# Performance work log

Measured on AMD Instinct MI355X. Metric: run time of the kernel, lower is better.

## Reference

```python
import jax, jax.numpy as jnp
import numpy as np

EMBED = 512
HEADS = 8
HEAD_D = EMBED // HEADS
N = 16
QLEN = 512
KLEN = 512


def _relative_keys(Wr, q_len, k_len):
    # Transformer-XL style sinusoid table of size (q_len + k_len)
    max_dist = q_len + k_len
    inv_freqs = 10000.0 ** (-jnp.arange(0, EMBED, 2, dtype=jnp.float32) / EMBED)
    seq = jnp.arange(max_dist, dtype=jnp.float32)[:, None] * inv_freqs[None, :]
    pos_emb = jnp.concatenate([jnp.sin(seq), jnp.cos(seq)], axis=-1)  # [max_dist, E]
    rel = (pos_emb @ Wr.T).reshape(max_dist, HEADS, HEAD_D)           # [max_dist, H, D]
    # query_offset defaults to key_len
    q_pos = jnp.arange(q_len)[:, None] + k_len
    k_pos = jnp.arange(k_len)[None, :]
    rel_idx = jnp.clip(q_pos - k_pos, 0, max_dist - 1)                # [q, k]
    return rel[rel_idx]                                               # [q, k, H, D]


def setup_inputs() -> dict:
    key = jax.random.key(0)
    ks = jax.random.split(key, 12)
    s = 0.02
    return {
        "values": jax.random.normal(ks[0], (N, KLEN, EMBED), jnp.float32),
        "keys": jax.random.normal(ks[1], (N, KLEN, EMBED), jnp.float32),
        "query": jax.random.normal(ks[2], (N, QLEN, EMBED), jnp.float32),
        "mask": jnp.ones((N, QLEN, KLEN), jnp.int32),
        "Wv": jax.random.normal(ks[3], (HEAD_D, HEAD_D), jnp.float32) * s,
        "Wk": jax.random.normal(ks[4], (HEAD_D, HEAD_D), jnp.float32) * s,
        "Wq": jax.random.normal(ks[5], (HEAD_D, HEAD_D), jnp.float32) * s,
        "Wr": jax.random.normal(ks[6], (EMBED, EMBED), jnp.float32) * s,
        "u_bias": jax.random.normal(ks[7], (HEADS, HEAD_D), jnp.float32) * s,
        "v_bias": jax.random.normal(ks[8], (HEADS, HEAD_D), jnp.float32) * s,
        "Wo": jax.random.normal(ks[9], (EMBED, EMBED), jnp.float32) * s,
        "bo": jnp.zeros((EMBED,), jnp.float32),
    }


def reference(values, keys, query, mask, Wv, Wk, Wq, Wr, u_bias, v_bias, Wo, bo):
    # per-head projections (same D x D weight shared across heads, torch Linear: x @ W.T)
    v = values.reshape(N, KLEN, HEADS, HEAD_D) @ Wv.T
    k = keys.reshape(N, KLEN, HEADS, HEAD_D) @ Wk.T
    q = query.reshape(N, QLEN, HEADS, HEAD_D) @ Wq.T

    rel_keys = _relative_keys(Wr, QLEN, KLEN)  # [q, k, H, D]

    content = jnp.einsum("nqhd,nkhd->nhqk", q + u_bias, k)
    position = jnp.einsum("nqhd,qkhd->nhqk", q + v_bias, rel_keys)
    energy = content + position
    energy = jnp.where(mask[:, None, :, :] == 0, jnp.float32(-1e20), energy)

    attn = jax.nn.softmax(energy / (float(HEAD_D) ** 0.5), axis=3)  # [N,H,q,k]
    out = jnp.einsum("nhqk,nkhd->nqhd", attn, v).reshape(N, QLEN, EMBED)
    out = out @ Wo.T + bo
    return out, attn
```

## Files before the change

kernel.cpp:

```cpp
#include <hip/hip_runtime.h>
#include <math.h>

#define NB     16
#define HEADS  8
#define HD     64
#define EMBED  512
#define QL     512
#define KL     512

#define WS_QU   0
#define WS_QV   2097152
#define WS_KB   4194304
#define WS_VT   6291456
#define WS_PEB  8388608
#define WS_RELB 8912896
#define WS_OH   9175040

typedef __attribute__((ext_vector_type(8))) short bf16x8;
typedef __attribute__((ext_vector_type(4))) float f32x4;
typedef __attribute__((ext_vector_type(8))) unsigned short ushort8v;
typedef __attribute__((ext_vector_type(4))) unsigned short ushort4v;

#define MFMA16 __builtin_amdgcn_mfma_f32_16x16x32_bf16

static __device__ __forceinline__ unsigned short f2bf(float x) {
    unsigned u = __builtin_bit_cast(unsigned, x);
    u += 0x7fffu + ((u >> 16) & 1u);
    return (unsigned short)(u >> 16);
}

static __device__ __forceinline__ float bf2f(unsigned short v) {
    unsigned u = ((unsigned)v) << 16;
    return __builtin_bit_cast(float, u);
}

__global__ void pe_kernel(unsigned short* __restrict__ peb) {
    int j = blockIdx.x;
    int i = threadIdx.x;
    float invf = exp2f(-(float)i * (13.287712379549449f / 256.0f));
    float ang  = (float)j * invf;
    peb[j * 512 + i]       = f2bf(sinf(ang));
    peb[j * 512 + 256 + i] = f2bf(cosf(ang));
}

__global__ __launch_bounds__(256) void rel_kernel(const unsigned short* __restrict__ peb,
                                                  const float* __restrict__ Wr,
                                                  unsigned short* __restrict__ relb) {
    __shared__ __align__(16) unsigned short At[64][64];
    __shared__ __align__(16) unsigned short Bt[64][64];
    int bm = blockIdx.x >> 3, bn = blockIdx.x & 7;
    int tid = threadIdx.x;
    int w = tid >> 6, lane = tid & 63;
    int fr = lane & 15, fg = lane >> 4;
    f32x4 acc[4] = {};
    for (int kk = 0; kk < 512; kk += 64) {
        __syncthreads();
        for (int p = 0; p < 2; ++p) {
            int idx = tid + 256 * p;
            int row = idx >> 3, slot = idx & 7;
            *(bf16x8*)&At[row][((slot ^ (row & 7))) * 8] =
                *(const bf16x8*)&peb[(bm * 64 + row) * 512 + kk + slot * 8];
        }
        for (int p = 0; p < 4; ++p) {
            int idx = tid + 256 * p;
            int row = idx >> 4, c4 = idx & 15;
            float4 v = *(const float4*)&Wr[(bn * 64 + row) * 512 + kk + c4 * 4];
            ushort4v pk;
            pk[0] = f2bf(v.x); pk[1] = f2bf(v.y); pk[2] = f2bf(v.z); pk[3] = f2bf(v.w);
            int slot = c4 >> 1, rem = (c4 & 1) * 4;
            *(ushort4v*)&Bt[row][((slot ^ (row & 7))) * 8 + rem] = pk;
        }
        __syncthreads();
        bf16x8 af[2];
        int ar = w * 16 + fr;
#pragma unroll
        for (int s = 0; s < 2; ++s)
            af[s] = *(const bf16x8*)&At[ar][((fg + 4 * s) ^ (ar & 7)) * 8];
#pragma unroll
        for (int c = 0; c < 4; ++c) {
            int br = c * 16 + fr;
#pragma unroll
            for (int s = 0; s < 2; ++s) {
                bf16x8 bf = *(const bf16x8*)&Bt[br][((fg + 4 * s) ^ (br & 7)) * 8];
                acc[c] = MFMA16(af[s], bf, acc[c], 0, 0, 0);
            }
        }
    }
#pragma unroll
    for (int c = 0; c < 4; ++c)
#pragma unroll
        for (int i = 0; i < 4; ++i)
            relb[(bn * 1024 + bm * 64 + w * 16 + fg * 4 + i) * 64 + c * 16 + fr] =
                f2bf(acc[c][i]);
}

__global__ __launch_bounds__(256) void proj_kernel(const float* __restrict__ query,
                                                   const float* __restrict__ keys,
                                                   const float* __restrict__ values,
                                                   const float* __restrict__ Wq,
                                                   const float* __restrict__ Wk,
                                                   const float* __restrict__ Wv,
                                                   const float* __restrict__ u_bias,
                                                   const float* __restrict__ v_bias,
                                                   float* __restrict__ ws) {
    __shared__ __align__(16) unsigned short inb[32][512];
    __shared__ __align__(16) unsigned short Wb[3][64][64];
    __shared__ __align__(16) unsigned short vtile[4][64][36];
    int n = blockIdx.x >> 4, t0 = (blockIdx.x & 15) * 32;
    int tid = threadIdx.x;
    int w = tid >> 6, lane = tid & 63;
    int fr = lane & 15, fg = lane >> 4;

    for (int p = 0; p < 3; ++p) {
        const float* Wp = (p == 0) ? Wq : (p == 1) ? Wk : Wv;
        for (int it = 0; it < 4; ++it) {
            int idx = tid + 256 * it;
            int row = idx >> 4, c4 = idx & 15;
            float4 v = *(const float4*)&Wp[row * 64 + c4 * 4];
            ushort4v pk;
            pk[0] = f2bf(v.x); pk[1] = f2bf(v.y); pk[2] = f2bf(v.z); pk[3] = f2bf(v.w);
            int slot = c4 >> 1, rem = (c4 & 1) * 4;
            *(ushort4v*)&Wb[p][row][((slot ^ (row & 7))) * 8 + rem] = pk;
        }
    }
    unsigned short* qu_b = (unsigned short*)(ws + WS_QU);
    unsigned short* qv_b = (unsigned short*)(ws + WS_QV);
    unsigned short* k_b  = (unsigned short*)(ws + WS_KB);
    unsigned short* vT_b = (unsigned short*)(ws + WS_VT);

    for (int p = 0; p < 3; ++p) {
        const float* src = (p == 0) ? query : (p == 1) ? keys : values;
        __syncthreads();
        for (int it = 0; it < 16; ++it) {
            int idx = tid + 256 * it;
            int row = idx >> 7, c4 = idx & 127;
            float4 v = *(const float4*)&src[((long)(n * 512 + t0 + row)) * 512 + c4 * 4];
            ushort4v pk;
            pk[0] = f2bf(v.x); pk[1] = f2bf(v.y); pk[2] = f2bf(v.z); pk[3] = f2bf(v.w);
            int slot = c4 >> 1, rem = (c4 & 1) * 4;
            *(ushort4v*)&inb[row][((slot ^ (row & 7))) * 8 + rem] = pk;
        }
        __syncthreads();
        for (int hh = 0; hh < 2; ++hh) {
            int h = w * 2 + hh, nh = n * 8 + h;
            bf16x8 af[2][2];
#pragma unroll
            for (int tt = 0; tt < 2; ++tt) {
                int ar = tt * 16 + fr;
#pragma unroll
                for (int s = 0; s < 2; ++s)
                    af[tt][s] = *(const bf16x8*)&inb[ar][(h * 8 + ((fg + 4 * s) ^ (ar & 7))) * 8];
            }
            f32x4 acc[2][4] = {};
#pragma unroll
            for (int dt = 0; dt < 4; ++dt) {
                int br = dt * 16 + fr;
                bf16x8 bf[2];
#pragma unroll
                for (int s = 0; s < 2; ++s)
                    bf[s] = *(const bf16x8*)&Wb[p][br][((fg + 4 * s) ^ (br & 7)) * 8];
#pragma unroll
                for (int tt = 0; tt < 2; ++tt)
#pragma unroll
                    for (int s = 0; s < 2; ++s)
                        acc[tt][dt] = MFMA16(af[tt][s], bf[s], acc[tt][dt], 0, 0, 0);
            }
            if (p == 0) {
#pragma unroll
                for (int dt = 0; dt < 4; ++dt) {
                    float ub = u_bias[h * 64 + dt * 16 + fr];
                    float vb = v_bias[h * 64 + dt * 16 + fr];
#pragma unroll
                    for (int tt = 0; tt < 2; ++tt)
#pragma unroll
                        for (int i = 0; i < 4; ++i) {
                            long o = ((long)(nh * 512 + t0 + tt * 16 + fg * 4 + i)) * 64 +
                                     dt * 16 + fr;
                            qu_b[o] = f2bf(acc[tt][dt][i] + ub);
                            qv_b[o] = f2bf(acc[tt][dt][i] + vb);
                        }
                }
            } else if (p == 1) {
#pragma unroll
                for (int dt = 0; dt < 4; ++dt)
#pragma unroll
                    for (int tt = 0; tt < 2; ++tt)
#pragma unroll
                        for (int i = 0; i < 4; ++i)
                            k_b[((long)(nh * 512 + t0 + tt * 16 + fg * 4 + i)) * 64 +
                                dt * 16 + fr] = f2bf(acc[tt][dt][i]);
            } else {
#pragma unroll
                for (int dt = 0; dt < 4; ++dt)
#pragma unroll
                    for (int tt = 0; tt < 2; ++tt)
#pragma unroll
                        for (int i = 0; i < 4; ++i)
                            vtile[w][dt * 16 + fr][tt * 16 + fg * 4 + i] =
                                f2bf(acc[tt][dt][i]);
                __syncthreads();
#pragma unroll
                for (int dg = 0; dg < 8; ++dg) {
                    int d = dg * 8 + (lane >> 3), tq = lane & 7;
                    *(ushort4v*)&vT_b[((long)(nh * 64 + d)) * 512 + t0 + tq * 4] =
                        *(const ushort4v*)&vtile[w][d][tq * 4];
                }
                __syncthreads();
            }
        }
    }
}

__global__ __launch_bounds__(512) void attn_kernel(float* __restrict__ ws,
                                                   const int* __restrict__ mask,
                                                   float* __restrict__ d_out) {
    __shared__ __align__(16) float S[32][520];
    __shared__ __align__(16) float red[4][32][17];

    const unsigned short* qu_b = (const unsigned short*)(ws + WS_QU);
    const unsigned short* qv_b = (const unsigned short*)(ws + WS_QV);
    const unsigned short* k_b  = (const unsigned short*)(ws + WS_KB);
    const unsigned short* vT_b = (const unsigned short*)(ws + WS_VT);
    const unsigned short* relb = (const unsigned short*)(ws + WS_RELB);
    unsigned short* ohb = (unsigned short*)(ws + WS_OH);
    float* attn = d_out + 4194304;

    int bid = blockIdx.x;
    int swz = (bid & 7) * 128 + (bid >> 3);
    int nh = swz >> 3, qg = swz & 7;
    int n  = nh >> 3, h = nh & 7;

    int tid  = threadIdx.x;
    int w    = tid >> 6, lane = tid & 63;
    int fr   = lane & 15, fg = lane >> 4;

    const unsigned short* kbase = k_b + (long)nh * 512 * 64;
    bf16x8 kreg[4][2];
#pragma unroll
    for (int t = 0; t < 4; ++t) {
        const unsigned short* kp = kbase + (long)(w * 64 + t * 16 + fr) * 64;
        kreg[t][0] = *(const bf16x8*)&kp[fg * 8];
        kreg[t][1] = *(const bf16x8*)&kp[(fg + 4) * 8];
    }
    int dt = w & 3, kh = w >> 2;
    const unsigned short* vp0 = vT_b + ((long)(nh * 64 + dt * 16 + fr)) * 512 + kh * 256;
    bf16x8 vreg[8];
#pragma unroll
    for (int kk = 0; kk < 8; ++kk)
        vreg[kk] = *(const bf16x8*)&vp0[kk * 32 + fg * 8];

    const unsigned short* rbase = relb + (long)h * 1024 * 64;
    int jt0 = 28 - 4 * w;

    for (int ti = 0; ti < 2; ++ti) {
        int q0 = qg * 64 + ti * 32;

        {
            bf16x8 qvf[2][2];
#pragma unroll
            for (int qt = 0; qt < 2; ++qt) {
                long qa = ((long)(nh * 512 + q0 + qt * 16 + fr)) * 64;
                qvf[qt][0] = *(const bf16x8*)&qv_b[qa + fg * 8];
                qvf[qt][1] = *(const bf16x8*)&qv_b[qa + (fg + 4) * 8];
            }
#pragma unroll
            for (int pp = 0; pp < 3; ++pp) {
                int jjA = (jt0 + 2 * pp) * 16 + fr;
                int jjB = jjA + 16;
                int jA = q0 + 1 + jjA; if (jA > 1023) jA = 1023;
                int jB = q0 + 1 + jjB; if (jB > 1023) jB = 1023;
                const unsigned short* rpA = rbase + (long)jA * 64;
                const unsigned short* rpB = rbase + (long)jB * 64;
                bf16x8 a0 = *(const bf16x8*)&rpA[fg * 8];
                bf16x8 a1 = *(const bf16x8*)&rpA[(fg + 4) * 8];
                bf16x8 c0 = *(const bf16x8*)&rpB[fg * 8];
                bf16x8 c1 = *(const bf16x8*)&rpB[(fg + 4) * 8];
                __builtin_amdgcn_s_setprio(1);
#pragma unroll
                for (int qt = 0; qt < 2; ++qt) {
                    f32x4 accA = {0.f, 0.f, 0.f, 0.f};
                    f32x4 accB = {0.f, 0.f, 0.f, 0.f};
                    accA = MFMA16(qvf[qt][0], a0, accA, 0, 0, 0);
                    accA = MFMA16(qvf[qt][1], a1, accA, 0, 0, 0);
                    accB = MFMA16(qvf[qt][0], c0, accB, 0, 0, 0);
                    accB = MFMA16(qvf[qt][1], c1, accB, 0, 0, 0);
#pragma unroll
                    for (int i = 0; i < 4; ++i) {
                        int r = qt * 16 + fg * 4 + i;
                        int kA = r + 511 - jjA;
                        int kB = r + 511 - jjB;
                        if ((unsigned)(kA - w * 64) < 64u)
                            S[r][kA ^ (4 * (r & 7))] = accA[i];
                        if ((unsigned)(kB - w * 64) < 64u)
                            S[r][kB ^ (4 * (r & 7))] = accB[i];
                    }
                }
                __builtin_amdgcn_s_setprio(0);
            }
        }

        {
            bf16x8 qf[2][2];
#pragma unroll
            for (int qt = 0; qt < 2; ++qt) {
                long qa = ((long)(nh * 512 + q0 + qt * 16 + fr)) * 64;
                qf[qt][0] = *(const bf16x8*)&qu_b[qa + fg * 8];
                qf[qt][1] = *(const bf16x8*)&qu_b[qa + (fg + 4) * 8];
            }
            __builtin_amdgcn_s_setprio(1);
#pragma unroll
            for (int t = 0; t < 4; ++t) {
#pragma unroll
                for (int qt = 0; qt < 2; ++qt) {
                    f32x4* sp = (f32x4*)&S[qt * 16 + fr]
                                        [(w * 64 + t * 16 + fg * 4) ^ (4 * (fr & 7))];
                    f32x4 acc = *sp;
                    acc = MFMA16(kreg[t][0], qf[qt][0], acc, 0, 0, 0);
                    acc = MFMA16(kreg[t][1], qf[qt][1], acc, 0, 0, 0);
                    *sp = acc;
                }
            }
            __builtin_amdgcn_s_setprio(0);
        }
        __syncthreads();

        for (int rr = 0; rr < 4; ++rr) {
            int r = w * 4 + rr;
            int x4 = 4 * (r & 7), x8 = 8 * (r & 7);
            const int* mrow = mask + ((long)(n * 512 + q0 + r)) * 512;
            float lg[8];
            float mx = -3.0e38f;
#pragma unroll
            for (int j = 0; j < 8; ++j) {
                int k = lane + 64 * j;
                float s = S[r][k ^ x4];
                int m = mrow[k];
                float l = (m == 0) ? -1.25e19f : s * 0.125f;
                lg[j] = l;
                mx = fmaxf(mx, l);
            }
            for (int o = 32; o > 0; o >>= 1) mx = fmaxf(mx, __shfl_xor(mx, o, 64));
            float sum = 0.f;
#pragma unroll
            for (int j = 0; j < 8; ++j) { lg[j] = __expf(lg[j] - mx); sum += lg[j]; }
            for (int o = 32; o > 0; o >>= 1) sum += __shfl_xor(sum, o, 64);
            float inv = 1.0f / sum;
            unsigned short* prow = (unsigned short*)&S[r][0];
            float* arow = attn + ((long)(nh * 512 + q0 + r)) * 512;
#pragma unroll
            for (int j = 0; j < 8; ++j) {
                int k = lane + 64 * j;
                float p = lg[j] * inv;
                prow[k ^ x8] = f2bf(p);
                arow[k] = p;
            }
        }
        __syncthreads();

        {
            f32x4 oacc[2] = {{0.f,0.f,0.f,0.f},{0.f,0.f,0.f,0.f}};
            __builtin_amdgcn_s_setprio(1);
#pragma unroll
            for (int kk = 0; kk < 8; ++kk) {
#pragma unroll
                for (int qt = 0; qt < 2; ++qt) {
                    int row = qt * 16 + fr;
                    const unsigned short* prow = (const unsigned short*)&S[row][0];
                    bf16x8 pf = *(const bf16x8*)
                        &prow[(kh * 256 + kk * 32 + fg * 8) ^ (8 * (row & 7))];
                    oacc[qt] = MFMA16(pf, vreg[kk], oacc[qt], 0, 0, 0);
                }
            }
            __builtin_amdgcn_s_setprio(0);
            if (kh == 1) {
#pragma unroll
                for (int qt = 0; qt < 2; ++qt)
#pragma unroll
                    for (int i = 0; i < 4; ++i)
                        red[dt][qt * 16 + fg * 4 + i][fr] = oacc[qt][i];
            }
            __syncthreads();
            if (kh == 0) {
#pragma unroll
                for (int qt = 0; qt < 2; ++qt)
#pragma unroll
                    for (int i = 0; i < 4; ++i) {
                        float o = oacc[qt][i] + red[dt][qt * 16 + fg * 4 + i][fr];
                        ohb[((long)(n * 512 + q0 + qt * 16 + fg * 4 + i)) * 512 +
                            h * 64 + dt * 16 + fr] = f2bf(o);
                    }
            }
        }
    }
}

__global__ __launch_bounds__(256) void wo_kernel(const float* __restrict__ ws,
                                                 const float* __restrict__ Wo,
                                                 const float* __restrict__ bo,
                                                 float* __restrict__ d_out) {
    __shared__ __align__(16) unsigned short At[128][64];
    __shared__ __align__(16) unsigned short Bt[64][64];
    const unsigned short* ohb = (const unsigned short*)(ws + WS_OH);
    int bm = blockIdx.x >> 3, bn = blockIdx.x & 7;
    int tid = threadIdx.x;
    int w = tid >> 6, lane = tid & 63;
    int fr = lane & 15, fg = lane >> 4;
    f32x4 acc[2][4] = {};
    for (int kk = 0; kk < 512; kk += 64) {
        __syncthreads();
        for (int p = 0; p < 4; ++p) {
            int idx = tid + 256 * p;
            int row = idx >> 3, slot = idx & 7;
            *(bf16x8*)&At[row][((slot ^ (row & 7))) * 8] =
                *(const bf16x8*)&ohb[(long)(bm * 128 + row) * 512 + kk + slot * 8];
        }
        for (int p = 0; p < 2; ++p) {
            int idx = tid + 256 * p;
            int row = idx >> 3, slot = idx & 7;
            const float* g = &Wo[(bn * 64 + row) * 512 + kk + slot * 8];
            float4 a = *(const float4*)g;
            float4 b = *(const float4*)(g + 4);
            ushort8v pk;
            pk[0] = f2bf(a.x); pk[1] = f2bf(a.y); pk[2] = f2bf(a.z); pk[3] = f2bf(a.w);
            pk[4] = f2bf(b.x); pk[5] = f2bf(b.y); pk[6] = f2bf(b.z); pk[7] = f2bf(b.w);
            *(ushort8v*)&Bt[row][((slot ^ (row & 7))) * 8] = pk;
        }
        __syncthreads();
        bf16x8 af[2][2], bfr[4][2];
#pragma unroll
        for (int t = 0; t < 2; ++t) {
            int ar = w * 32 + t * 16 + fr;
#pragma unroll
            for (int s = 0; s < 2; ++s)
                af[t][s] = *(const bf16x8*)&At[ar][((fg + s * 4) ^ (ar & 7)) * 8];
        }
#pragma unroll
        for (int c = 0; c < 4; ++c) {
            int br = c * 16 + fr;
#pragma unroll
            for (int s = 0; s < 2; ++s)
                bfr[c][s] = *(const bf16x8*)&Bt[br][((fg + s * 4) ^ (br & 7)) * 8];
        }
#pragma unroll
        for (int t = 0; t < 2; ++t)
#pragma unroll
            for (int c = 0; c < 4; ++c)
#pragma unroll
                for (int s = 0; s < 2; ++s)
                    acc[t][c] = MFMA16(af[t][s], bfr[c][s], acc[t][c], 0, 0, 0);
    }
#pragma unroll
    for (int t = 0; t < 2; ++t)
#pragma unroll
        for (int c = 0; c < 4; ++c) {
            int col = bn * 64 + c * 16 + fr;
            float b = bo[col];
#pragma unroll
            for (int i = 0; i < 4; ++i) {
                int row = bm * 128 + w * 32 + t * 16 + fg * 4 + i;
                d_out[(long)row * 512 + col] = acc[t][c][i] + b;
            }
        }
}

extern "C" void kernel_launch(void* const* d_in, const int* in_sizes, int n_in,
                              void* d_out, int out_size, void* d_ws, size_t ws_size,
                              hipStream_t stream) {
    const float* values = (const float*)d_in[0];
    const float* keys   = (const float*)d_in[1];
    const float* query  = (const float*)d_in[2];
    const int*   mask   = (const int*)d_in[3];
    const float* Wv     = (const float*)d_in[4];
    const float* Wk     = (const float*)d_in[5];
    const float* Wq     = (const float*)d_in[6];
    const float* Wr     = (const float*)d_in[7];
    const float* u_bias = (const float*)d_in[8];
    const float* v_bias = (const float*)d_in[9];
    const float* Wo     = (const float*)d_in[10];
    const float* bo     = (const float*)d_in[11];
    float* out = (float*)d_out;
    float* ws  = (float*)d_ws;

    unsigned short* peb  = (unsigned short*)(ws + WS_PEB);
    unsigned short* relb = (unsigned short*)(ws + WS_RELB);

    hipLaunchKernelGGL(pe_kernel,   dim3(1024),  dim3(256), 0, stream, peb);
    hipLaunchKernelGGL(rel_kernel,  dim3(128),   dim3(256), 0, stream, peb, Wr, relb);
    hipLaunchKernelGGL(proj_kernel, dim3(256),   dim3(256), 0, stream,
                       query, keys, values, Wq, Wk, Wv, u_bias, v_bias, ws);
    hipLaunchKernelGGL(attn_kernel, dim3(1024),  dim3(512), 0, stream, ws, mask, out);
    hipLaunchKernelGGL(wo_kernel,   dim3(512),   dim3(256), 0, stream, ws, Wo, bo, out);
}
```

Measured before the change: 157.6 us.

## Double-buffer bf16 score tiles and overlap PV with next tile's scores

Result: no change. 158.2 us (+0.4%).

```diff
diff --git a/kernel.cpp b/kernel.cpp
--- a/kernel.cpp
+++ b/kernel.cpp
@@ -32,6 +32,15 @@
 static __device__ __forceinline__ float bf2f(unsigned short v) {
     unsigned u = ((unsigned)v) << 16;
     return __builtin_bit_cast(float, u);
+}
+
+static __device__ __forceinline__ bf16x8 pack8(f32x4 a, f32x4 b) {
+    union { bf16x8 v; unsigned u[4]; } r;
+    asm("v_cvt_pk_bf16_f32 %0, %1, %2" : "=v"(r.u[0]) : "v"(a[0]), "v"(a[1]));
+    asm("v_cvt_pk_bf16_f32 %0, %1, %2" : "=v"(r.u[1]) : "v"(a[2]), "v"(a[3]));
+    asm("v_cvt_pk_bf16_f32 %0, %1, %2" : "=v"(r.u[2]) : "v"(b[0]), "v"(b[1]));
+    asm("v_cvt_pk_bf16_f32 %0, %1, %2" : "=v"(r.u[3]) : "v"(b[2]), "v"(b[3]));
+    return r.v;
 }
 
 __global__ void pe_kernel(unsigned short* __restrict__ peb) {
@@ -214,7 +223,7 @@
 __global__ __launch_bounds__(512) void attn_kernel(float* __restrict__ ws,
                                                    const int* __restrict__ mask,
                                                    float* __restrict__ d_out) {
-    __shared__ __align__(16) float S[32][520];
+    __shared__ __align__(16) unsigned short S16[2][32][528];
     __shared__ __align__(16) float red[4][32][17];
 
     const unsigned short* qu_b = (const unsigned short*)(ws + WS_QU);
@@ -252,146 +261,160 @@
     const unsigned short* rbase = relb + (long)h * 1024 * 64;
     int jt0 = 28 - 4 * w;
 
-    for (int ti = 0; ti < 2; ++ti) {
-        int q0 = qg * 64 + ti * 32;
-
-        {
-            bf16x8 qvf[2][2];
+    auto pos_content = [&](int q0, unsigned short (*SB)[528]) {
+        bf16x8 qf[2][2], qv[2][2];
+#pragma unroll
+        for (int qt = 0; qt < 2; ++qt) {
+            long qa = ((long)(nh * 512 + q0 + qt * 16 + fr)) * 64;
+            qf[qt][0] = *(const bf16x8*)&qu_b[qa + fg * 8];
+            qf[qt][1] = *(const bf16x8*)&qu_b[qa + (fg + 4) * 8];
+            qv[qt][0] = *(const bf16x8*)&qv_b[qa + fg * 8];
+            qv[qt][1] = *(const bf16x8*)&qv_b[qa + (fg + 4) * 8];
+        }
+#pragma unroll
+        for (int pp = 0; pp < 3; ++pp) {
+            int jtA = jt0 + 2 * pp, jtB = jtA + 1;
+            int jA = q0 + 1 + jtA * 16 + fr; if (jA > 1023) jA = 1023;
+            int jB = q0 + 1 + jtB * 16 + fr; if (jB > 1023) jB = 1023;
+            const unsigned short* rpA = rbase + (long)jA * 64;
+            const unsigned short* rpB = rbase + (long)jB * 64;
+            bf16x8 a0 = *(const bf16x8*)&rpA[fg * 8];
+            bf16x8 a1 = *(const bf16x8*)&rpA[(fg + 4) * 8];
+            bf16x8 c0 = *(const bf16x8*)&rpB[fg * 8];
+            bf16x8 c1 = *(const bf16x8*)&rpB[(fg + 4) * 8];
+            __builtin_amdgcn_s_setprio(1);
 #pragma unroll
             for (int qt = 0; qt < 2; ++qt) {
-                long qa = ((long)(nh * 512 + q0 + qt * 16 + fr)) * 64;
-                qvf[qt][0] = *(const bf16x8*)&qv_b[qa + fg * 8];
-                qvf[qt][1] = *(const bf16x8*)&qv_b[qa + (fg + 4) * 8];
-            }
-#pragma unroll
-            for (int pp = 0; pp < 3; ++pp) {
-                int jjA = (jt0 + 2 * pp) * 16 + fr;
-                int jjB = jjA + 16;
-                int jA = q0 + 1 + jjA; if (jA > 1023) jA = 1023;
-                int jB = q0 + 1 + jjB; if (jB > 1023) jB = 1023;
-                const unsigned short* rpA = rbase + (long)jA * 64;
-                const unsigned short* rpB = rbase + (long)jB * 64;
-                bf16x8 a0 = *(const bf16x8*)&rpA[fg * 8];
-                bf16x8 a1 = *(const bf16x8*)&rpA[(fg + 4) * 8];
-                bf16x8 c0 = *(const bf16x8*)&rpB[fg * 8];
-                bf16x8 c1 = *(const bf16x8*)&rpB[(fg + 4) * 8];
-                __builtin_amdgcn_s_setprio(1);
-#pragma unroll
-                for (int qt = 0; qt < 2; ++qt) {
-                    f32x4 accA = {0.f, 0.f, 0.f, 0.f};
-                    f32x4 accB = {0.f, 0.f, 0.f, 0.f};
-                    accA = MFMA16(qvf[qt][0], a0, accA, 0, 0, 0);
-                    accA = MFMA16(qvf[qt][1], a1, accA, 0, 0, 0);
-                    accB = MFMA16(qvf[qt][0], c0, accB, 0, 0, 0);
-                    accB = MFMA16(qvf[qt][1], c1, accB, 0, 0, 0);
-#pragma unroll
-                    for (int i = 0; i < 4; ++i) {
-                        int r = qt * 16 + fg * 4 + i;
-                        int kA = r + 511 - jjA;
-                        int kB = r + 511 - jjB;
-                        if ((unsigned)(kA - w * 64) < 64u)
-                            S[r][kA ^ (4 * (r & 7))] = accA[i];
-                        if ((unsigned)(kB - w * 64) < 64u)
-                            S[r][kB ^ (4 * (r & 7))] = accB[i];
-                    }
+                f32x4 accA = {0.f, 0.f, 0.f, 0.f};
+                f32x4 accB = {0.f, 0.f, 0.f, 0.f};
+                accA = MFMA16(a0, qv[qt][0], accA, 0, 0, 0);
+                accA = MFMA16(a1, qv[qt][1], accA, 0, 0, 0);
+                accB = MFMA16(c0, qv[qt][0], accB, 0, 0, 0);
+                accB = MFMA16(c1, qv[qt][1], accB, 0, 0, 0);
+                int qr = qt * 16 + fr;
+                int x8 = 8 * (fr & 7);
+#pragma unroll
+                for (int i = 0; i < 4; ++i) {
+                    int kA = qr + 511 - (jtA * 16 + fg * 4 + i);
+                    int kB = qr + 511 - (jtB * 16 + fg * 4 + i);
+                    if ((unsigned)(kA - w * 64) < 64u)
+                        SB[qr][kA ^ x8] = f2bf(accA[i]);
+                    if ((unsigned)(kB - w * 64) < 64u)
+                        SB[qr][kB ^ x8] = f2bf(accB[i]);
                 }
-                __builtin_amdgcn_s_setprio(0);
-            }
-        }
-
-        {
-            bf16x8 qf[2][2];
+            }
+            __builtin_amdgcn_s_setprio(0);
+        }
+        __builtin_amdgcn_s_setprio(1);
+#pragma unroll
+        for (int t = 0; t < 4; ++t) {
 #pragma unroll
             for (int qt = 0; qt < 2; ++qt) {
-                long qa = ((long)(nh * 512 + q0 + qt * 16 + fr)) * 64;
-                qf[qt][0] = *(const bf16x8*)&qu_b[qa + fg * 8];
-                qf[qt][1] = *(const bf16x8*)&qu_b[qa + (fg + 4) * 8];
-            }
-            __builtin_amdgcn_s_setprio(1);
-#pragma unroll
-            for (int t = 0; t < 4; ++t) {
-#pragma unroll
-                for (int qt = 0; qt < 2; ++qt) {
-                    f32x4* sp = (f32x4*)&S[qt * 16 + fr]
-                                        [(w * 64 + t * 16 + fg * 4) ^ (4 * (fr & 7))];
-                    f32x4 acc = *sp;
-                    acc = MFMA16(kreg[t][0], qf[qt][0], acc, 0, 0, 0);
-                    acc = MFMA16(kreg[t][1], qf[qt][1], acc, 0, 0, 0);
-                    *sp = acc;
-                }
-            }
-            __builtin_amdgcn_s_setprio(0);
-        }
-        __syncthreads();
-
+                int qr = qt * 16 + fr;
+                unsigned short* sp =
+                    &SB[qr][(w * 64 + t * 16 + fg * 4) ^ (8 * (fr & 7))];
+                ushort4v cv = *(ushort4v*)sp;
+                f32x4 cin = {bf2f(cv[0]), bf2f(cv[1]), bf2f(cv[2]), bf2f(cv[3])};
+                cin = MFMA16(kreg[t][0], qf[qt][0], cin, 0, 0, 0);
+                cin = MFMA16(kreg[t][1], qf[qt][1], cin, 0, 0, 0);
+                ushort4v ov;
+                ov[0] = f2bf(cin[0]); ov[1] = f2bf(cin[1]);
+                ov[2] = f2bf(cin[2]); ov[3] = f2bf(cin[3]);
+                *(ushort4v*)sp = ov;
+            }
+        }
+        __builtin_amdgcn_s_setprio(0);
+    };
+
+    auto softmax_f = [&](int q0, unsigned short (*SB)[528]) {
         for (int rr = 0; rr < 4; ++rr) {
             int r = w * 4 + rr;
-            int x4 = 4 * (r & 7), x8 = 8 * (r & 7);
-            const int* mrow = mask + ((long)(n * 512 + q0 + r)) * 512;
+            int slot = lane ^ (r & 7);
+            bf16x8 sv = *(const bf16x8*)&SB[r][slot * 8];
+            const int* mrow = mask + ((long)(n * 512 + q0 + r)) * 512 + lane * 8;
+            int4 m0 = *(const int4*)mrow;
+            int4 m1 = *(const int4*)(mrow + 4);
+            int mv[8] = {m0.x, m0.y, m0.z, m0.w, m1.x, m1.y, m1.z, m1.w};
             float lg[8];
             float mx = -3.0e38f;
 #pragma unroll
-            for (int j = 0; j < 8; ++j) {
-                int k = lane + 64 * j;
-                float s = S[r][k ^ x4];
-                int m = mrow[k];
-                float l = (m == 0) ? -1.25e19f : s * 0.125f;
-                lg[j] = l;
+            for (int u = 0; u < 8; ++u) {
+                float sraw = bf2f((unsigned short)sv[u]);
+                float l = (mv[u] == 0) ? -1.25e19f : sraw * 0.125f;
+                lg[u] = l;
                 mx = fmaxf(mx, l);
             }
             for (int o = 32; o > 0; o >>= 1) mx = fmaxf(mx, __shfl_xor(mx, o, 64));
             float sum = 0.f;
 #pragma unroll
-            for (int j = 0; j < 8; ++j) { lg[j] = __expf(lg[j] - mx); sum += lg[j]; }
+            for (int u = 0; u < 8; ++u) { lg[u] = __expf(lg[u] - mx); sum += lg[u]; }
             for (int o = 32; o > 0; o >>= 1) sum += __shfl_xor(sum, o, 64);
             float inv = 1.0f / sum;
-            unsigned short* prow = (unsigned short*)&S[r][0];
-            float* arow = attn + ((long)(nh * 512 + q0 + r)) * 512;
-#pragma unroll
-            for (int j = 0; j < 8; ++j) {
-                int k = lane + 64 * j;
-                float p = lg[j] * inv;
-                prow[k ^ x8] = f2bf(p);
-                arow[k] = p;
-            }
-        }
-        __syncthreads();
-
-        {
-            f32x4 oacc[2] = {{0.f,0.f,0.f,0.f},{0.f,0.f,0.f,0.f}};
-            __builtin_amdgcn_s_setprio(1);
-#pragma unroll
-            for (int kk = 0; kk < 8; ++kk) {
-#pragma unroll
-                for (int qt = 0; qt < 2; ++qt) {
-                    int row = qt * 16 + fr;
-                    const unsigned short* prow = (const unsigned short*)&S[row][0];
-                    bf16x8 pf = *(const bf16x8*)
-                        &prow[(kh * 256 + kk * 32 + fg * 8) ^ (8 * (row & 7))];
-                    oacc[qt] = MFMA16(pf, vreg[kk], oacc[qt], 0, 0, 0);
+            f32x4 p0 = {lg[0] * inv, lg[1] * inv, lg[2] * inv, lg[3] * inv};
+            f32x4 p1 = {lg[4] * inv, lg[5] * inv, lg[6] * inv, lg[7] * inv};
+            *(bf16x8*)&SB[r][slot * 8] = pack8(p0, p1);
+            float* arow = attn + ((long)(nh * 512 + q0 + r)) * 512 + lane * 8;
+            *(f32x4*)arow = p0;
+            *(f32x4*)(arow + 4) = p1;
+        }
+    };
+
+    auto pv = [&](unsigned short (*SB)[528], f32x4* oacc) {
+        __builtin_amdgcn_s_setprio(1);
+#pragma unroll
+        for (int kk = 0; kk < 8; ++kk) {
+#pragma unroll
+            for (int qt = 0; qt < 2; ++qt) {
+                int row = qt * 16 + fr;
+                bf16x8 pf = *(const bf16x8*)
+                    &SB[row][(kh * 256 + kk * 32 + fg * 8) ^ (8 * (fr & 7))];
+                oacc[qt] = MFMA16(pf, vreg[kk], oacc[qt], 0, 0, 0);
+            }
+        }
+        __builtin_amdgcn_s_setprio(0);
+    };
+
+    auto red_write = [&](f32x4* oacc) {
+        if (kh == 1) {
+#pragma unroll
+            for (int qt = 0; qt < 2; ++qt)
+#pragma unroll
+                for (int i = 0; i < 4; ++i)
+                    red[dt][qt * 16 + fg * 4 + i][fr] = oacc[qt][i];
+        }
+    };
+    auto red_read_store = [&](int q0, f32x4* oacc) {
+        if (kh == 0) {
+#pragma unroll
+            for (int qt = 0; qt < 2; ++qt)
+#pragma unroll
+                for (int i = 0; i < 4; ++i) {
+                    float o = oacc[qt][i] + red[dt][qt * 16 + fg * 4 + i][fr];
+                    ohb[((long)(n * 512 + q0 + qt * 16 + fg * 4 + i)) * 512 +
+                        h * 64 + dt * 16 + fr] = f2bf(o);
                 }
-            }
-            __builtin_amdgcn_s_setprio(0);
-            if (kh == 1) {
-#pragma unroll
-                for (int qt = 0; qt < 2; ++qt)
-#pragma unroll
-                    for (int i = 0; i < 4; ++i)
-                        red[dt][qt * 16 + fg * 4 + i][fr] = oacc[qt][i];
-            }
-            __syncthreads();
-            if (kh == 0) {
-#pragma unroll
-                for (int qt = 0; qt < 2; ++qt)
-#pragma unroll
-                    for (int i = 0; i < 4; ++i) {
-                        float o = oacc[qt][i] + red[dt][qt * 16 + fg * 4 + i][fr];
-                        ohb[((long)(n * 512 + q0 + qt * 16 + fg * 4 + i)) * 512 +
-                            h * 64 + dt * 16 + fr] = f2bf(o);
-                    }
-            }
-        }
-    }
+        }
+    };
+
+    int q0a = qg * 64, q0b = qg * 64 + 32;
+
+    pos_content(q0a, S16[0]);
+    __syncthreads();
+    softmax_f(q0a, S16[0]);
+    __syncthreads();
+    f32x4 oacc0[2] = {{0.f,0.f,0.f,0.f},{0.f,0.f,0.f,0.f}};
+    pv(S16[0], oacc0);
+    pos_content(q0b, S16[1]);
+    red_write(oacc0);
+    __syncthreads();
+    red_read_store(q0a, oacc0);
+    softmax_f(q0b, S16[1]);
+    __syncthreads();
+    f32x4 oacc1[2] = {{0.f,0.f,0.f,0.f},{0.f,0.f,0.f,0.f}};
+    pv(S16[1], oacc1);
+    red_write(oacc1);
+    __syncthreads();
+    red_read_store(q0b, oacc1);
 }
 
 __global__ __launch_bounds__(256) void wo_kernel(const float* __restrict__ ws,
```
